# Kernel tuning notes

Hardware: AMD Instinct MI355X
Metric: run time of the kernel (lower is better)

## Reference

```python
import jax, jax.numpy as jnp
import numpy as np

NUM_PITCHES = 88
H_FEAT = 188
LSTM_UNITS = 48
N_STATES = 5
CTX_HID = 16
CTX_OUT = 4


def _glorot(key, shape):
    fan_in, fan_out = shape[1], shape[0]
    lim = (6.0 / (fan_in + fan_out)) ** 0.5
    return jax.random.uniform(key, shape, jnp.float32, -lim, lim)


def setup_inputs() -> dict:
    key = jax.random.key(0)
    ks = jax.random.split(key, 16)
    B, T = 16, 256
    pitch_features = jax.random.normal(ks[0], (B, NUM_PITCHES, H_FEAT, T), jnp.float32)
    prev_context = jax.random.uniform(ks[1], (B, NUM_PITCHES, 3), jnp.float32)
    # context net params
    fc1_w = _glorot(ks[2], (CTX_HID, 3)); fc1_b = jnp.zeros((CTX_HID,), jnp.float32)
    fc2_w = _glorot(ks[3], (CTX_HID, CTX_HID)); fc2_b = jnp.zeros((CTX_HID,), jnp.float32)
    fc3_w = _glorot(ks[4], (CTX_OUT, CTX_HID)); fc3_b = jnp.zeros((CTX_OUT,), jnp.float32)
    # lstm1: input H_FEAT+4 -> 48; gates order i,f,g,o (torch convention)
    in1 = H_FEAT + CTX_OUT
    lstm1_wih = _glorot(ks[5], (4 * LSTM_UNITS, in1))
    lstm1_whh = _glorot(ks[6], (4 * LSTM_UNITS, LSTM_UNITS))
    lstm1_bih = jnp.zeros((4 * LSTM_UNITS,), jnp.float32)
    lstm1_bhh = jnp.zeros((4 * LSTM_UNITS,), jnp.float32)
    lstm2_wih = _glorot(ks[7], (4 * LSTM_UNITS, LSTM_UNITS))
    lstm2_whh = _glorot(ks[8], (4 * LSTM_UNITS, LSTM_UNITS))
    lstm2_bih = jnp.zeros((4 * LSTM_UNITS,), jnp.float32)
    lstm2_bhh = jnp.zeros((4 * LSTM_UNITS,), jnp.float32)
    fc_states_w = _glorot(ks[9], (N_STATES, LSTM_UNITS))
    fc_states_b = jnp.zeros((N_STATES,), jnp.float32)
    return dict(pitch_features=pitch_features, prev_context=prev_context,
                fc1_w=fc1_w, fc1_b=fc1_b, fc2_w=fc2_w, fc2_b=fc2_b,
                fc3_w=fc3_w, fc3_b=fc3_b,
                lstm1_wih=lstm1_wih, lstm1_whh=lstm1_whh, lstm1_bih=lstm1_bih, lstm1_bhh=lstm1_bhh,
                lstm2_wih=lstm2_wih, lstm2_whh=lstm2_whh, lstm2_bih=lstm2_bih, lstm2_bhh=lstm2_bhh,
                fc_states_w=fc_states_w, fc_states_b=fc_states_b)


def _lstm_scan(x, wih, whh, bih, bhh):
    # x: (S, N, In); zero init state; returns (S, N, U)
    S, N, _ = x.shape
    U = whh.shape[1]
    xg = jnp.einsum('sni,gi->sng', x, wih) + bih + bhh  # precompute input gates

    def step(carry, xg_t):
        h, c = carry
        g = xg_t + h @ whh.T  # (N, 4U)
        i, f, gg, o = jnp.split(g, 4, axis=-1)
        c = jax.nn.sigmoid(f) * c + jax.nn.sigmoid(i) * jnp.tanh(gg)
        h = jax.nn.sigmoid(o) * jnp.tanh(c)
        return (h, c), h

    init = (jnp.zeros((N, U), x.dtype), jnp.zeros((N, U), x.dtype))
    _, hs = jax.lax.scan(step, init, xg)
    return hs


def reference(pitch_features, prev_context,
              fc1_w, fc1_b, fc2_w, fc2_b, fc3_w, fc3_b,
              lstm1_wih, lstm1_whh, lstm1_bih, lstm1_bhh,
              lstm2_wih, lstm2_whh, lstm2_bih, lstm2_bhh,
              fc_states_w, fc_states_b):
    B, P, H, T = pitch_features.shape
    # Context net (context never updates across t in the original loop)
    x = jax.nn.relu(prev_context @ fc1_w.T + fc1_b)
    x = jax.nn.relu(x @ fc2_w.T + fc2_b)
    ctx_emb = x @ fc3_w.T + fc3_b  # (B, P, 4)
    # Each timestep t is independent: LSTM runs over the pitch axis (len 88)
    # with zero initial state every step. Fold (B, T) into batch N.
    pf = jnp.transpose(pitch_features, (1, 0, 3, 2)).reshape(P, B * T, H)  # (P, BT, H)
    ce = jnp.broadcast_to(ctx_emb[:, None, :, :], (B, T, P, CTX_OUT))
    ce = jnp.transpose(ce, (2, 0, 1, 3)).reshape(P, B * T, CTX_OUT)
    seq = jnp.concatenate([pf, ce], axis=-1)  # (P, BT, H+4)
    h = _lstm_scan(seq, lstm1_wih, lstm1_whh, lstm1_bih, lstm1_bhh)
    h = _lstm_scan(h, lstm2_wih, lstm2_whh, lstm2_bih, lstm2_bhh)
    logits = h @ fc_states_w.T + fc_states_b  # (P, BT, 5)
    logits = logits.reshape(P, B, T, N_STATES)
    logits = jnp.transpose(logits, (1, 0, 3, 2))  # (B, P, 5, T)
    return jax.nn.softmax(logits, axis=2)
```

## Files before the change

kernel.cpp:

```cpp
#include <hip/hip_runtime.h>
#include <hip/hip_bf16.h>
#include <cstdint>

#define P_ 88
#define B_ 16
#define T_ 256
#define H_ 188
#define G_ 192
#define U_ 48
#define N_ 4096

typedef __attribute__((ext_vector_type(8))) short bf16x8;
typedef __attribute__((ext_vector_type(8))) _Float16 f16x8;
typedef __attribute__((ext_vector_type(4))) float f32x4;

__device__ __forceinline__ float sigf(float x) {
  return __builtin_amdgcn_rcpf(1.0f + __expf(-x));
}
__device__ __forceinline__ float tanh_f(float x) {
  return 1.0f - 2.0f * __builtin_amdgcn_rcpf(1.0f + __expf(2.0f * x));
}
__device__ __forceinline__ unsigned short f2bs(float v) {
  union { __hip_bfloat16 h; unsigned short s; } u;
  u.h = __float2bfloat16(v);
  return u.s;
}
__device__ __forceinline__ float bs2f(unsigned short s) {
  union { unsigned int u; float f; } x;
  x.u = ((unsigned int)s) << 16;
  return x.f;
}
__device__ __forceinline__ float hs2f(unsigned short s) {
  union { unsigned short u; _Float16 h; } x;
  x.u = s;
  return (float)x.h;
}
__device__ __forceinline__ unsigned short f2hs(float v) {
  union { _Float16 h; unsigned short s; } x;
  x.h = (_Float16)v;
  return x.s;
}

__device__ __forceinline__ void lds_barrier() {
  asm volatile("s_waitcnt lgkmcnt(0)\n\ts_barrier" ::: "memory");
}

__global__ void ctx_kernel(const float* __restrict__ pc,
                           const float* __restrict__ fc1w, const float* __restrict__ fc1b,
                           const float* __restrict__ fc2w, const float* __restrict__ fc2b,
                           const float* __restrict__ fc3w, const float* __restrict__ fc3b,
                           const float* __restrict__ wih1,
                           const float* __restrict__ bih1, const float* __restrict__ bhh1,
                           float* __restrict__ ctxg) {
  int bp = blockIdx.x * 64 + threadIdx.x;
  if (bp >= B_ * P_) return;
  float p0 = pc[bp * 3 + 0], p1 = pc[bp * 3 + 1], p2 = pc[bp * 3 + 2];
  float x1[16], x2[16];
#pragma unroll
  for (int jj = 0; jj < 16; ++jj)
    x1[jj] = fmaxf(0.f, fc1w[jj * 3 + 0] * p0 + fc1w[jj * 3 + 1] * p1 + fc1w[jj * 3 + 2] * p2 + fc1b[jj]);
#pragma unroll
  for (int jj = 0; jj < 16; ++jj) {
    float s = fc2b[jj];
#pragma unroll
    for (int i = 0; i < 16; ++i) s += fc2w[jj * 16 + i] * x1[i];
    x2[jj] = fmaxf(0.f, s);
  }
  float ce[4];
#pragma unroll
  for (int jj = 0; jj < 4; ++jj) {
    float s = fc3b[jj];
#pragma unroll
    for (int i = 0; i < 16; ++i) s += fc3w[jj * 16 + i] * x2[i];
    ce[jj] = s;
  }
  float* op = ctxg + (size_t)bp * G_;
  for (int g = 0; g < G_; ++g) {
    const float* wr = wih1 + (size_t)g * G_ + H_;
    op[g] = bih1[g] + bhh1[g] + ce[0] * wr[0] + ce[1] * wr[1] + ce[2] * wr[2] + ce[3] * wr[3];
  }
}

__global__ __launch_bounds__(256) void wfrag_kernel(const float* __restrict__ wih1,
                                                    f16x8* __restrict__ wfrag) {
  const int idx = blockIdx.x * 256 + threadIdx.x;
  if (idx >= 12 * 6 * 64) return;
  const int l = idx & 63;
  const int kc = (idx >> 6) % 6;
  const int j = idx / 384;
  const int g = j * 16 + (l & 15);
  const int k0 = kc * 32 + (l >> 4) * 8;
  f16x8 v;
#pragma unroll
  for (int e = 0; e < 8; ++e) {
    const int k = k0 + e;
    const float wv = (k < H_) ? wih1[(size_t)g * G_ + k] : 0.f;
    v[e] = (_Float16)wv;
  }
  wfrag[idx] = v;
}

__global__ __launch_bounds__(256, 3) void gemm_mfma(const float* __restrict__ pf,
                                                    const f16x8* __restrict__ wfrag,
                                                    const float* __restrict__ ctxg,
                                                    unsigned short* __restrict__ xg2) {
  const int bp = blockIdx.x >> 1, tb = blockIdx.x & 1;
  const int p = bp % P_, b = bp / P_;
  const int tid = threadIdx.x;
  const int w = tid >> 6, l = tid & 63;
  const int lj = l & 15, lq = l >> 4;

  __shared__ __align__(16) char ldsraw[49152];
  _Float16(*Ahi)[34] = (_Float16(*)[34])ldsraw;
  _Float16(*Alo)[34] = (_Float16(*)[34])(ldsraw + 8704);

  float cg[12];
#pragma unroll
  for (int jn = 0; jn < 12; ++jn)
    cg[jn] = ctxg[(size_t)bp * G_ + jn * 16 + lj];

  f32x4 acc[2][12];
#pragma unroll
  for (int mt = 0; mt < 2; ++mt)
#pragma unroll
    for (int jn = 0; jn < 12; ++jn)
#pragma unroll
      for (int r = 0; r < 4; ++r) acc[mt][jn][r] = 0.f;

  const float* Ab = pf + (size_t)bp * H_ * T_ + tb * 128;
  const int kl = tid >> 5;
  const int t4 = (tid & 31) * 4;

  for (int kc = 0; kc < 6; ++kc) {
    __syncthreads();
#pragma unroll
    for (int rr = 0; rr < 4; ++rr) {
      const int kk = rr * 8 + kl;
      const int kg = kc * 32 + kk;
      float a0 = 0.f, a1 = 0.f, a2 = 0.f, a3 = 0.f;
      if (kg < H_) {
        const float4 v = *(const float4*)(Ab + (size_t)kg * T_ + t4);
        a0 = v.x; a1 = v.y; a2 = v.z; a3 = v.w;
      }
      const _Float16 h0 = (_Float16)a0, h1 = (_Float16)a1;
      const _Float16 h2 = (_Float16)a2, h3 = (_Float16)a3;
      Ahi[t4 + 0][kk] = h0; Alo[t4 + 0][kk] = (_Float16)(a0 - (float)h0);
      Ahi[t4 + 1][kk] = h1; Alo[t4 + 1][kk] = (_Float16)(a1 - (float)h1);
      Ahi[t4 + 2][kk] = h2; Alo[t4 + 2][kk] = (_Float16)(a2 - (float)h2);
      Ahi[t4 + 3][kk] = h3; Alo[t4 + 3][kk] = (_Float16)(a3 - (float)h3);
    }
    __syncthreads();
    const int trow = w * 32;
    const f16x8 ahi0 = *(const f16x8*)&Ahi[trow + lj][lq * 8];
    const f16x8 ahi1 = *(const f16x8*)&Ahi[trow + 16 + lj][lq * 8];
    const f16x8 alo0 = *(const f16x8*)&Alo[trow + lj][lq * 8];
    const f16x8 alo1 = *(const f16x8*)&Alo[trow + 16 + lj][lq * 8];
#pragma unroll
    for (int jn = 0; jn < 12; ++jn) {
      const f16x8 wf = wfrag[(jn * 6 + kc) * 64 + l];
      acc[0][jn] = __builtin_amdgcn_mfma_f32_16x16x32_f16(ahi0, wf, acc[0][jn], 0, 0, 0);
      acc[1][jn] = __builtin_amdgcn_mfma_f32_16x16x32_f16(ahi1, wf, acc[1][jn], 0, 0, 0);
      acc[0][jn] = __builtin_amdgcn_mfma_f32_16x16x32_f16(alo0, wf, acc[0][jn], 0, 0, 0);
      acc[1][jn] = __builtin_amdgcn_mfma_f32_16x16x32_f16(alo1, wf, acc[1][jn], 0, 0, 0);
    }
  }
  __syncthreads();

  unsigned short* Cst = (unsigned short*)ldsraw + w * 6144;
#pragma unroll
  for (int mt = 0; mt < 2; ++mt)
#pragma unroll
    for (int jn = 0; jn < 12; ++jn)
#pragma unroll
      for (int r = 0; r < 4; ++r)
        Cst[mt * 3072 + jn * 256 + r * 64 + l] = f2hs(acc[mt][jn][r] + cg[jn]);
  const int nb0 = b * 16 + tb * 8 + w * 2;
  unsigned short* gb = xg2 + ((size_t)p * 256 + nb0) * 3072;
#pragma unroll
  for (int rr = 0; rr < 12; ++rr) {
    const uint4 v = *(const uint4*)(Cst + rr * 512 + l * 8);
    *(uint4*)(gb + rr * 512 + l * 8) = v;
  }
}

__global__ __launch_bounds__(256, 2) void scan_mfma(
    const unsigned short* __restrict__ xg2,
    const float* __restrict__ whh1, const float* __restrict__ wih2,
    const float* __restrict__ whh2, const float* __restrict__ bih2,
    const float* __restrict__ bhh2, const float* __restrict__ fcw,
    const float* __restrict__ fcb, float* __restrict__ out) {
  __shared__ __align__(16) short hh[16][104];
  __shared__ __align__(16) short hl[16][104];
  __shared__ __align__(16) float gs[8][196];
  __shared__ __align__(16) float h2f[8][52];
  __shared__ __align__(16) float fcws[5 * 48];
  __shared__ float logit_s[5][8];
  __shared__ float prob_s[5][8];

  const int tid = threadIdx.x;
  const int w = tid >> 6;
  const int l = tid & 63;
  const int lj = l & 15;
  const int lq = l >> 4;
  const int grp = blockIdx.x >> 1;
  const int half = blockIdx.x & 1;
  const int n0 = blockIdx.x * 8;
  const int b = n0 >> 8, t0 = n0 & 255;

  bf16x8 b1[3][2];
  bf16x8 b2f[3][3];
  float bias2r[3];
#pragma unroll
  for (int i = 0; i < 3; ++i) {
    const int j = w * 48 + i * 16 + lj;
    bias2r[i] = bih2[j] + bhh2[j];
#pragma unroll
    for (int kc = 0; kc < 2; ++kc)
#pragma unroll
      for (int e = 0; e < 8; ++e) {
        const int u = kc * 32 + lq * 8 + e;
        b1[i][kc][e] = (u < U_) ? (short)f2bs(whh1[j * U_ + u]) : (short)0;
      }
#pragma unroll
    for (int kc = 0; kc < 3; ++kc)
#pragma unroll
      for (int e = 0; e < 8; ++e) {
        const int u = kc * 32 + lq * 8 + e;
        b2f[i][kc][e] = (u < U_) ? (short)f2bs(wih2[j * U_ + u])
                                 : (short)f2bs(whh2[j * U_ + (u - U_)]);
      }
  }

  for (int e = tid; e < 16 * 104 / 2; e += 256) {
    ((unsigned int*)hh)[e] = 0u;
    ((unsigned int*)hl)[e] = 0u;
  }
  for (int e = tid; e < 5 * U_; e += 256) fcws[e] = fcw[e];

  const int tn0 = tid / U_, tu0 = tid % U_;
  const int tn1 = (256 + tid) / U_, tu1 = (256 + tid) % U_;
  float c1r[2] = {0.f, 0.f}, c2r[2] = {0.f, 0.f};
  const bool fcth = tid < 40;
  const int fk = tid >> 3, fn = tid & 7;
  const float fcbr = fcth ? fcb[fk] : 0.f;
  const int sk = (tid - 96) >> 3, sn = (tid - 96) & 7;

  unsigned short xp[12];
  {
    const size_t pb = (size_t)grp * 3072;
#pragma unroll
    for (int i = 0; i < 3; ++i)
#pragma unroll
      for (int r = 0; r < 4; ++r)
        xp[i * 4 + r] = (lq < 2)
            ? xg2[pb + (size_t)((w * 3 + i) * 256 + r * 64 + (half * 2 + lq) * 16 + lj)]
            : (unsigned short)0;
  }
  const short* hhrow = &hh[lj][0];
  const short* hlrow = &hl[lj][0];
  lds_barrier();

  for (int p = 0; p < P_; ++p) {
    f32x4 cH[3], cL[3];
#pragma unroll
    for (int i = 0; i < 3; ++i)
#pragma unroll
      for (int r = 0; r < 4; ++r) { cH[i][r] = hs2f(xp[i * 4 + r]); cL[i][r] = 0.f; }
    if (p < P_ - 1) {
      const size_t pb = (size_t)((p + 1) * 256 + grp) * 3072;
#pragma unroll
      for (int i = 0; i < 3; ++i)
#pragma unroll
        for (int r = 0; r < 4; ++r)
          xp[i * 4 + r] = (lq < 2)
              ? xg2[pb + (size_t)((w * 3 + i) * 256 + r * 64 + (half * 2 + lq) * 16 + lj)]
              : (unsigned short)0;
    }
    {
      bf16x8 ah0 = *(const bf16x8*)(hhrow + lq * 8);
      bf16x8 ah1 = *(const bf16x8*)(hhrow + 32 + lq * 8);
      bf16x8 al0 = *(const bf16x8*)(hlrow + lq * 8);
      bf16x8 al1 = *(const bf16x8*)(hlrow + 32 + lq * 8);
#pragma unroll
      for (int i = 0; i < 3; ++i)
        cH[i] = __builtin_amdgcn_mfma_f32_16x16x32_bf16(ah0, b1[i][0], cH[i], 0, 0, 0);
#pragma unroll
      for (int i = 0; i < 3; ++i)
        cL[i] = __builtin_amdgcn_mfma_f32_16x16x32_bf16(al0, b1[i][0], cL[i], 0, 0, 0);
#pragma unroll
      for (int i = 0; i < 3; ++i)
        cH[i] = __builtin_amdgcn_mfma_f32_16x16x32_bf16(ah1, b1[i][1], cH[i], 0, 0, 0);
#pragma unroll
      for (int i = 0; i < 3; ++i)
        cL[i] = __builtin_amdgcn_mfma_f32_16x16x32_bf16(al1, b1[i][1], cL[i], 0, 0, 0);
    }
    if (lq < 2) {
#pragma unroll
      for (int i = 0; i < 3; ++i)
#pragma unroll
        for (int r = 0; r < 4; ++r)
          gs[lq * 4 + r][w * 48 + i * 16 + lj] = cH[i][r] + cL[i][r];
    }
    if (p > 0 && fcth) {
      float a = fcbr;
#pragma unroll
      for (int uq = 0; uq < 12; ++uq) {
        f32x4 hv = *(const f32x4*)&h2f[fn][uq * 4];
        f32x4 wv = *(const f32x4*)&fcws[fk * 48 + uq * 4];
        a += hv[0] * wv[0] + hv[1] * wv[1] + hv[2] * wv[2] + hv[3] * wv[3];
      }
      logit_s[fk][fn] = a;
    }
    lds_barrier();
    {
      const int n = tn0, u = tu0;
      const float ig = gs[n][u], fg = gs[n][48 + u];
      const float gg = gs[n][96 + u], og = gs[n][144 + u];
      const float cc = sigf(fg) * c1r[0] + sigf(ig) * tanh_f(gg);
      c1r[0] = cc;
      const float h = sigf(og) * tanh_f(cc);
      const unsigned short hb = f2bs(h);
      hh[n][u] = (short)hb;
      hl[n][u] = (short)f2bs(h - bs2f(hb));
    }
    if (tid < 128) {
      const int n = tn1, u = tu1;
      const float ig = gs[n][u], fg = gs[n][48 + u];
      const float gg = gs[n][96 + u], og = gs[n][144 + u];
      const float cc = sigf(fg) * c1r[1] + sigf(ig) * tanh_f(gg);
      c1r[1] = cc;
      const float h = sigf(og) * tanh_f(cc);
      const unsigned short hb = f2bs(h);
      hh[n][u] = (short)hb;
      hl[n][u] = (short)f2bs(h - bs2f(hb));
    }
    if (p > 0 && tid >= 192 && tid < 200) {
      const int n = tid - 192;
      const float l0 = logit_s[0][n], l1 = logit_s[1][n], l2 = logit_s[2][n],
                  l3 = logit_s[3][n], l4 = logit_s[4][n];
      const float m = fmaxf(fmaxf(fmaxf(l0, l1), fmaxf(l2, l3)), l4);
      const float e0 = __expf(l0 - m), e1 = __expf(l1 - m), e2 = __expf(l2 - m),
                  e3 = __expf(l3 - m), e4 = __expf(l4 - m);
      const float rs = __builtin_amdgcn_rcpf(e0 + e1 + e2 + e3 + e4);
      prob_s[0][n] = e0 * rs; prob_s[1][n] = e1 * rs; prob_s[2][n] = e2 * rs;
      prob_s[3][n] = e3 * rs; prob_s[4][n] = e4 * rs;
    }
    lds_barrier();
    f32x4 c2H[3], c2L[3];
#pragma unroll
    for (int i = 0; i < 3; ++i) {
      c2H[i][0] = bias2r[i]; c2H[i][1] = bias2r[i];
      c2H[i][2] = bias2r[i]; c2H[i][3] = bias2r[i];
      c2L[i][0] = 0.f; c2L[i][1] = 0.f; c2L[i][2] = 0.f; c2L[i][3] = 0.f;
    }
    {
      bf16x8 a0 = *(const bf16x8*)(hhrow + lq * 8);
      bf16x8 a1 = *(const bf16x8*)(hhrow + 32 + lq * 8);
      bf16x8 a2 = *(const bf16x8*)(hhrow + 64 + lq * 8);
      bf16x8 q0 = *(const bf16x8*)(hlrow + lq * 8);
      bf16x8 q1 = *(const bf16x8*)(hlrow + 32 + lq * 8);
      bf16x8 q2 = *(const bf16x8*)(hlrow + 64 + lq * 8);
#pragma unroll
      for (int i = 0; i < 3; ++i)
        c2H[i] = __builtin_amdgcn_mfma_f32_16x16x32_bf16(a0, b2f[i][0], c2H[i], 0, 0, 0);
#pragma unroll
      for (int i = 0; i < 3; ++i)
        c2L[i] = __builtin_amdgcn_mfma_f32_16x16x32_bf16(q0, b2f[i][0], c2L[i], 0, 0, 0);
#pragma unroll
      for (int i = 0; i < 3; ++i)
        c2H[i] = __builtin_amdgcn_mfma_f32_16x16x32_bf16(a1, b2f[i][1], c2H[i], 0, 0, 0);
#pragma unroll
      for (int i = 0; i < 3; ++i)
        c2L[i] = __builtin_amdgcn_mfma_f32_16x16x32_bf16(q1, b2f[i][1], c2L[i], 0, 0, 0);
#pragma unroll
      for (int i = 0; i < 3; ++i)
        c2H[i] = __builtin_amdgcn_mfma_f32_16x16x32_bf16(a2, b2f[i][2], c2H[i], 0, 0, 0);
#pragma unroll
      for (int i = 0; i < 3; ++i)
        c2L[i] = __builtin_amdgcn_mfma_f32_16x16x32_bf16(q2, b2f[i][2], c2L[i], 0, 0, 0);
    }
    if (lq < 2) {
#pragma unroll
      for (int i = 0; i < 3; ++i)
#pragma unroll
        for (int r = 0; r < 4; ++r)
          gs[lq * 4 + r][w * 48 + i * 16 + lj] = c2H[i][r] + c2L[i][r];
    }
    if (p > 0 && tid >= 96 && tid < 136) {
      out[(((size_t)b * P_ + (p - 1)) * 5 + sk) * T_ + t0 + sn] = prob_s[sk][sn];
    }
    lds_barrier();
    {
      const int n = tn0, u = tu0;
      const float ig = gs[n][u], fg = gs[n][48 + u];
      const float gg = gs[n][96 + u], og = gs[n][144 + u];
      const float cc = sigf(fg) * c2r[0] + sigf(ig) * tanh_f(gg);
      c2r[0] = cc;
      const float h = sigf(og) * tanh_f(cc);
      const unsigned short hb = f2bs(h);
      hh[n][48 + u] = (short)hb;
      hl[n][48 + u] = (short)f2bs(h - bs2f(hb));
      h2f[n][u] = h;
    }
    if (tid < 128) {
      const int n = tn1, u = tu1;
      const float ig = gs[n][u], fg = gs[n][48 + u];
      const float gg = gs[n][96 + u], og = gs[n][144 + u];
      const float cc = sigf(fg) * c2r[1] + sigf(ig) * tanh_f(gg);
      c2r[1] = cc;
      const float h = sigf(og) * tanh_f(cc);
      const unsigned short hb = f2bs(h);
      hh[n][48 + u] = (short)hb;
      hl[n][48 + u] = (short)f2bs(h - bs2f(hb));
      h2f[n][u] = h;
    }
    lds_barrier();
  }
  if (fcth) {
    float a = fcbr;
#pragma unroll
    for (int uq = 0; uq < 12; ++uq) {
      f32x4 hv = *(const f32x4*)&h2f[fn][uq * 4];
      f32x4 wv = *(const f32x4*)&fcws[fk * 48 + uq * 4];
      a += hv[0] * wv[0] + hv[1] * wv[1] + hv[2] * wv[2] + hv[3] * wv[3];
    }
    logit_s[fk][fn] = a;
  }
  lds_barrier();
  if (tid >= 192 && tid < 200) {
    const int n = tid - 192;
    const float l0 = logit_s[0][n], l1 = logit_s[1][n], l2 = logit_s[2][n],
                l3 = logit_s[3][n], l4 = logit_s[4][n];
    const float m = fmaxf(fmaxf(fmaxf(l0, l1), fmaxf(l2, l3)), l4);
    const float e0 = __expf(l0 - m), e1 = __expf(l1 - m), e2 = __expf(l2 - m),
                e3 = __expf(l3 - m), e4 = __expf(l4 - m);
    const float rs = __builtin_amdgcn_rcpf(e0 + e1 + e2 + e3 + e4);
    prob_s[0][n] = e0 * rs; prob_s[1][n] = e1 * rs; prob_s[2][n] = e2 * rs;
    prob_s[3][n] = e3 * rs; prob_s[4][n] = e4 * rs;
  }
  lds_barrier();
  if (tid >= 96 && tid < 136) {
    out[(((size_t)b * P_ + (P_ - 1)) * 5 + sk) * T_ + t0 + sn] = prob_s[sk][sn];
  }
}

extern "C" void kernel_launch(void* const* d_in, const int* in_sizes, int n_in,
                              void* d_out, int out_size, void* d_ws, size_t ws_size,
                              hipStream_t stream) {
  const float* pf   = (const float*)d_in[0];
  const float* pc   = (const float*)d_in[1];
  const float* fc1w = (const float*)d_in[2];
  const float* fc1b = (const float*)d_in[3];
  const float* fc2w = (const float*)d_in[4];
  const float* fc2b = (const float*)d_in[5];
  const float* fc3w = (const float*)d_in[6];
  const float* fc3b = (const float*)d_in[7];
  const float* wih1 = (const float*)d_in[8];
  const float* whh1 = (const float*)d_in[9];
  const float* bih1 = (const float*)d_in[10];
  const float* bhh1 = (const float*)d_in[11];
  const float* wih2 = (const float*)d_in[12];
  const float* whh2 = (const float*)d_in[13];
  const float* bih2 = (const float*)d_in[14];
  const float* bhh2 = (const float*)d_in[15];
  const float* fcw  = (const float*)d_in[16];
  const float* fcb  = (const float*)d_in[17];
  float* out = (float*)d_out;

  char* wsp = (char*)d_ws;
  float* ctxg = (float*)wsp;
  const size_t CTXG_BYTES = (size_t)B_ * P_ * G_ * sizeof(float);
  f16x8* wfrag = (f16x8*)(wsp + CTXG_BYTES);
  const size_t WFRAG_BYTES = (size_t)12 * 6 * 64 * 16;
  unsigned short* xg2 = (unsigned short*)(wsp + CTXG_BYTES + WFRAG_BYTES);

  ctx_kernel<<<22, 64, 0, stream>>>(pc, fc1w, fc1b, fc2w, fc2b, fc3w, fc3b,
                                    wih1, bih1, bhh1, ctxg);
  wfrag_kernel<<<18, 256, 0, stream>>>(wih1, wfrag);
  gemm_mfma<<<B_ * P_ * 2, 256, 0, stream>>>(pf, wfrag, ctxg, xg2);
  scan_mfma<<<N_ / 8, 256, 0, stream>>>(xg2, whh1, wih2, whh2,
                                        bih2, bhh2, fcw, fcb, out);
}
```

Before: 413.2 us.

## Skew two LSTM layers into one wavefront loop and drop bf16 hi/lo split

```diff
diff --git a/kernel.cpp b/kernel.cpp
--- a/kernel.cpp
+++ b/kernel.cpp
@@ -19,16 +19,6 @@
 }
 __device__ __forceinline__ float tanh_f(float x) {
   return 1.0f - 2.0f * __builtin_amdgcn_rcpf(1.0f + __expf(2.0f * x));
-}
-__device__ __forceinline__ unsigned short f2bs(float v) {
-  union { __hip_bfloat16 h; unsigned short s; } u;
-  u.h = __float2bfloat16(v);
-  return u.s;
-}
-__device__ __forceinline__ float bs2f(unsigned short s) {
-  union { unsigned int u; float f; } x;
-  x.u = ((unsigned int)s) << 16;
-  return x.f;
 }
 __device__ __forceinline__ float hs2f(unsigned short s) {
   union { unsigned short u; _Float16 h; } x;
@@ -189,9 +179,9 @@
     const float* __restrict__ whh2, const float* __restrict__ bih2,
     const float* __restrict__ bhh2, const float* __restrict__ fcw,
     const float* __restrict__ fcb, float* __restrict__ out) {
-  __shared__ __align__(16) short hh[16][104];
-  __shared__ __align__(16) short hl[16][104];
-  __shared__ __align__(16) float gs[8][196];
+  __shared__ __align__(16) _Float16 h12[16][104];
+  __shared__ __align__(16) float gs1[8][196];
+  __shared__ __align__(16) float gs2[8][196];
   __shared__ __align__(16) float h2f[8][52];
   __shared__ __align__(16) float fcws[5 * 48];
   __shared__ float logit_s[5][8];
@@ -207,8 +197,8 @@
   const int n0 = blockIdx.x * 8;
   const int b = n0 >> 8, t0 = n0 & 255;
 
-  bf16x8 b1[3][2];
-  bf16x8 b2f[3][3];
+  f16x8 b1[3][2];
+  f16x8 b2f[3][3];
   float bias2r[3];
 #pragma unroll
   for (int i = 0; i < 3; ++i) {
@@ -219,31 +209,33 @@
 #pragma unroll
       for (int e = 0; e < 8; ++e) {
         const int u = kc * 32 + lq * 8 + e;
-        b1[i][kc][e] = (u < U_) ? (short)f2bs(whh1[j * U_ + u]) : (short)0;
+        b1[i][kc][e] = (u < U_) ? (_Float16)whh1[j * U_ + u] : (_Float16)0.f;
       }
 #pragma unroll
     for (int kc = 0; kc < 3; ++kc)
 #pragma unroll
       for (int e = 0; e < 8; ++e) {
-        const int u = kc * 32 + lq * 8 + e;
-        b2f[i][kc][e] = (u < U_) ? (short)f2bs(wih2[j * U_ + u])
-                                 : (short)f2bs(whh2[j * U_ + (u - U_)]);
-      }
-  }
-
-  for (int e = tid; e < 16 * 104 / 2; e += 256) {
-    ((unsigned int*)hh)[e] = 0u;
-    ((unsigned int*)hl)[e] = 0u;
-  }
+        const int k = kc * 32 + lq * 8 + e;
+        b2f[i][kc][e] = (k < U_) ? (_Float16)wih2[j * U_ + k]
+                                 : (_Float16)whh2[j * U_ + (k - U_)];
+      }
+  }
+
+  for (int e = tid; e < 16 * 104 / 2; e += 256) ((unsigned int*)h12)[e] = 0u;
   for (int e = tid; e < 5 * U_; e += 256) fcws[e] = fcw[e];
 
   const int tn0 = tid / U_, tu0 = tid % U_;
   const int tn1 = (256 + tid) / U_, tu1 = (256 + tid) % U_;
-  float c1r[2] = {0.f, 0.f}, c2r[2] = {0.f, 0.f};
+  const bool has2 = (tid < 128);
+  float c1s[2] = {0.f, 0.f}, c2s[2] = {0.f, 0.f};
+
   const bool fcth = tid < 40;
   const int fk = tid >> 3, fn = tid & 7;
   const float fcbr = fcth ? fcb[fk] : 0.f;
+  const bool stth = tid >= 96 && tid < 136;
   const int sk = (tid - 96) >> 3, sn = (tid - 96) & 7;
+  const bool smth = tid >= 192 && tid < 200;
+  const int smn = tid - 192;
 
   unsigned short xp[12];
   {
@@ -256,52 +248,38 @@
             ? xg2[pb + (size_t)((w * 3 + i) * 256 + r * 64 + (half * 2 + lq) * 16 + lj)]
             : (unsigned short)0;
   }
-  const short* hhrow = &hh[lj][0];
-  const short* hlrow = &hl[lj][0];
   lds_barrier();
 
-  for (int p = 0; p < P_; ++p) {
-    f32x4 cH[3], cL[3];
-#pragma unroll
-    for (int i = 0; i < 3; ++i)
-#pragma unroll
-      for (int r = 0; r < 4; ++r) { cH[i][r] = hs2f(xp[i * 4 + r]); cL[i][r] = 0.f; }
-    if (p < P_ - 1) {
-      const size_t pb = (size_t)((p + 1) * 256 + grp) * 3072;
-#pragma unroll
-      for (int i = 0; i < 3; ++i)
-#pragma unroll
-        for (int r = 0; r < 4; ++r)
-          xp[i * 4 + r] = (lq < 2)
-              ? xg2[pb + (size_t)((w * 3 + i) * 256 + r * 64 + (half * 2 + lq) * 16 + lj)]
-              : (unsigned short)0;
-    }
-    {
-      bf16x8 ah0 = *(const bf16x8*)(hhrow + lq * 8);
-      bf16x8 ah1 = *(const bf16x8*)(hhrow + 32 + lq * 8);
-      bf16x8 al0 = *(const bf16x8*)(hlrow + lq * 8);
-      bf16x8 al1 = *(const bf16x8*)(hlrow + 32 + lq * 8);
-#pragma unroll
-      for (int i = 0; i < 3; ++i)
-        cH[i] = __builtin_amdgcn_mfma_f32_16x16x32_bf16(ah0, b1[i][0], cH[i], 0, 0, 0);
-#pragma unroll
-      for (int i = 0; i < 3; ++i)
-        cL[i] = __builtin_amdgcn_mfma_f32_16x16x32_bf16(al0, b1[i][0], cL[i], 0, 0, 0);
-#pragma unroll
-      for (int i = 0; i < 3; ++i)
-        cH[i] = __builtin_amdgcn_mfma_f32_16x16x32_bf16(ah1, b1[i][1], cH[i], 0, 0, 0);
-#pragma unroll
-      for (int i = 0; i < 3; ++i)
-        cL[i] = __builtin_amdgcn_mfma_f32_16x16x32_bf16(al1, b1[i][1], cL[i], 0, 0, 0);
-    }
-    if (lq < 2) {
-#pragma unroll
-      for (int i = 0; i < 3; ++i)
-#pragma unroll
-        for (int r = 0; r < 4; ++r)
-          gs[lq * 4 + r][w * 48 + i * 16 + lj] = cH[i][r] + cL[i][r];
-    }
-    if (p > 0 && fcth) {
+  for (int p = -1; p < P_; ++p) {
+    const _Float16* hr = &h12[lj][0];
+    const f16x8 f0 = *(const f16x8*)(hr + lq * 8);
+    const f16x8 f1 = *(const f16x8*)(hr + 32 + lq * 8);
+    const f16x8 f2 = *(const f16x8*)(hr + 64 + lq * 8);
+    if (p >= 0) {
+      f32x4 dH[3];
+#pragma unroll
+      for (int i = 0; i < 3; ++i) {
+        dH[i][0] = bias2r[i]; dH[i][1] = bias2r[i];
+        dH[i][2] = bias2r[i]; dH[i][3] = bias2r[i];
+      }
+#pragma unroll
+      for (int i = 0; i < 3; ++i)
+        dH[i] = __builtin_amdgcn_mfma_f32_16x16x32_f16(f0, b2f[i][0], dH[i], 0, 0, 0);
+#pragma unroll
+      for (int i = 0; i < 3; ++i)
+        dH[i] = __builtin_amdgcn_mfma_f32_16x16x32_f16(f1, b2f[i][1], dH[i], 0, 0, 0);
+#pragma unroll
+      for (int i = 0; i < 3; ++i)
+        dH[i] = __builtin_amdgcn_mfma_f32_16x16x32_f16(f2, b2f[i][2], dH[i], 0, 0, 0);
+      if (lq < 2) {
+#pragma unroll
+        for (int i = 0; i < 3; ++i)
+#pragma unroll
+          for (int r = 0; r < 4; ++r)
+            gs2[lq * 4 + r][w * 48 + i * 16 + lj] = dH[i][r];
+      }
+    }
+    if (p >= 1 && fcth) {
       float a = fcbr;
 #pragma unroll
       for (int uq = 0; uq < 12; ++uq) {
@@ -311,31 +289,83 @@
       }
       logit_s[fk][fn] = a;
     }
+    if (p >= 2 && stth) {
+      out[(((size_t)b * P_ + (p - 2)) * 5 + sk) * T_ + t0 + sn] = prob_s[sk][sn];
+    }
+    __builtin_amdgcn_sched_barrier(0);
+    if (p < P_ - 1) {
+      f32x4 cH[3];
+#pragma unroll
+      for (int i = 0; i < 3; ++i)
+#pragma unroll
+        for (int r = 0; r < 4; ++r) cH[i][r] = hs2f(xp[i * 4 + r]);
+      if (p < P_ - 2) {
+        const size_t pb = (size_t)((p + 2) * 256 + grp) * 3072;
+#pragma unroll
+        for (int i = 0; i < 3; ++i)
+#pragma unroll
+          for (int r = 0; r < 4; ++r)
+            xp[i * 4 + r] = (lq < 2)
+                ? xg2[pb + (size_t)((w * 3 + i) * 256 + r * 64 + (half * 2 + lq) * 16 + lj)]
+                : (unsigned short)0;
+      }
+#pragma unroll
+      for (int i = 0; i < 3; ++i)
+        cH[i] = __builtin_amdgcn_mfma_f32_16x16x32_f16(f0, b1[i][0], cH[i], 0, 0, 0);
+#pragma unroll
+      for (int i = 0; i < 3; ++i)
+        cH[i] = __builtin_amdgcn_mfma_f32_16x16x32_f16(f1, b1[i][1], cH[i], 0, 0, 0);
+      if (lq < 2) {
+#pragma unroll
+        for (int i = 0; i < 3; ++i)
+#pragma unroll
+          for (int r = 0; r < 4; ++r)
+            gs1[lq * 4 + r][w * 48 + i * 16 + lj] = cH[i][r];
+      }
+    }
     lds_barrier();
-    {
-      const int n = tn0, u = tu0;
-      const float ig = gs[n][u], fg = gs[n][48 + u];
-      const float gg = gs[n][96 + u], og = gs[n][144 + u];
-      const float cc = sigf(fg) * c1r[0] + sigf(ig) * tanh_f(gg);
-      c1r[0] = cc;
-      const float h = sigf(og) * tanh_f(cc);
-      const unsigned short hb = f2bs(h);
-      hh[n][u] = (short)hb;
-      hl[n][u] = (short)f2bs(h - bs2f(hb));
-    }
-    if (tid < 128) {
-      const int n = tn1, u = tu1;
-      const float ig = gs[n][u], fg = gs[n][48 + u];
-      const float gg = gs[n][96 + u], og = gs[n][144 + u];
-      const float cc = sigf(fg) * c1r[1] + sigf(ig) * tanh_f(gg);
-      c1r[1] = cc;
-      const float h = sigf(og) * tanh_f(cc);
-      const unsigned short hb = f2bs(h);
-      hh[n][u] = (short)hb;
-      hl[n][u] = (short)f2bs(h - bs2f(hb));
-    }
-    if (p > 0 && tid >= 192 && tid < 200) {
-      const int n = tid - 192;
+    if (p >= 0) {
+      {
+        const int n = tn0, u = tu0;
+        const float ig = gs2[n][u], fg = gs2[n][48 + u];
+        const float gg = gs2[n][96 + u], og = gs2[n][144 + u];
+        const float cc = sigf(fg) * c2s[0] + sigf(ig) * tanh_f(gg);
+        c2s[0] = cc;
+        const float h = sigf(og) * tanh_f(cc);
+        h12[n][48 + u] = (_Float16)h;
+        h2f[n][u] = h;
+      }
+      if (has2) {
+        const int n = tn1, u = tu1;
+        const float ig = gs2[n][u], fg = gs2[n][48 + u];
+        const float gg = gs2[n][96 + u], og = gs2[n][144 + u];
+        const float cc = sigf(fg) * c2s[1] + sigf(ig) * tanh_f(gg);
+        c2s[1] = cc;
+        const float h = sigf(og) * tanh_f(cc);
+        h12[n][48 + u] = (_Float16)h;
+        h2f[n][u] = h;
+      }
+    }
+    if (p < P_ - 1) {
+      {
+        const int n = tn0, u = tu0;
+        const float ig = gs1[n][u], fg = gs1[n][48 + u];
+        const float gg = gs1[n][96 + u], og = gs1[n][144 + u];
+        const float cc = sigf(fg) * c1s[0] + sigf(ig) * tanh_f(gg);
+        c1s[0] = cc;
+        h12[n][u] = (_Float16)(sigf(og) * tanh_f(cc));
+      }
+      if (has2) {
+        const int n = tn1, u = tu1;
+        const float ig = gs1[n][u], fg = gs1[n][48 + u];
+        const float gg = gs1[n][96 + u], og = gs1[n][144 + u];
+        const float cc = sigf(fg) * c1s[1] + sigf(ig) * tanh_f(gg);
+        c1s[1] = cc;
+        h12[n][u] = (_Float16)(sigf(og) * tanh_f(cc));
+      }
+    }
+    if (p >= 1 && smth) {
+      const int n = smn;
       const float l0 = logit_s[0][n], l1 = logit_s[1][n], l2 = logit_s[2][n],
                   l3 = logit_s[3][n], l4 = logit_s[4][n];
       const float m = fmaxf(fmaxf(fmaxf(l0, l1), fmaxf(l2, l3)), l4);
@@ -346,75 +376,6 @@
       prob_s[3][n] = e3 * rs; prob_s[4][n] = e4 * rs;
     }
     lds_barrier();
-    f32x4 c2H[3], c2L[3];
-#pragma unroll
-    for (int i = 0; i < 3; ++i) {
-      c2H[i][0] = bias2r[i]; c2H[i][1] = bias2r[i];
-      c2H[i][2] = bias2r[i]; c2H[i][3] = bias2r[i];
-      c2L[i][0] = 0.f; c2L[i][1] = 0.f; c2L[i][2] = 0.f; c2L[i][3] = 0.f;
-    }
-    {
-      bf16x8 a0 = *(const bf16x8*)(hhrow + lq * 8);
-      bf16x8 a1 = *(const bf16x8*)(hhrow + 32 + lq * 8);
-      bf16x8 a2 = *(const bf16x8*)(hhrow + 64 + lq * 8);
-      bf16x8 q0 = *(const bf16x8*)(hlrow + lq * 8);
-      bf16x8 q1 = *(const bf16x8*)(hlrow + 32 + lq * 8);
-      bf16x8 q2 = *(const bf16x8*)(hlrow + 64 + lq * 8);
-#pragma unroll
-      for (int i = 0; i < 3; ++i)
-        c2H[i] = __builtin_amdgcn_mfma_f32_16x16x32_bf16(a0, b2f[i][0], c2H[i], 0, 0, 0);
-#pragma unroll
-      for (int i = 0; i < 3; ++i)
-        c2L[i] = __builtin_amdgcn_mfma_f32_16x16x32_bf16(q0, b2f[i][0], c2L[i], 0, 0, 0);
-#pragma unroll
-      for (int i = 0; i < 3; ++i)
-        c2H[i] = __builtin_amdgcn_mfma_f32_16x16x32_bf16(a1, b2f[i][1], c2H[i], 0, 0, 0);
-#pragma unroll
-      for (int i = 0; i < 3; ++i)
-        c2L[i] = __builtin_amdgcn_mfma_f32_16x16x32_bf16(q1, b2f[i][1], c2L[i], 0, 0, 0);
-#pragma unroll
-      for (int i = 0; i < 3; ++i)
-        c2H[i] = __builtin_amdgcn_mfma_f32_16x16x32_bf16(a2, b2f[i][2], c2H[i], 0, 0, 0);
-#pragma unroll
-      for (int i = 0; i < 3; ++i)
-        c2L[i] = __builtin_amdgcn_mfma_f32_16x16x32_bf16(q2, b2f[i][2], c2L[i], 0, 0, 0);
-    }
-    if (lq < 2) {
-#pragma unroll
-      for (int i = 0; i < 3; ++i)
-#pragma unroll
-        for (int r = 0; r < 4; ++r)
-          gs[lq * 4 + r][w * 48 + i * 16 + lj] = c2H[i][r] + c2L[i][r];
-    }
-    if (p > 0 && tid >= 96 && tid < 136) {
-      out[(((size_t)b * P_ + (p - 1)) * 5 + sk) * T_ + t0 + sn] = prob_s[sk][sn];
-    }
-    lds_barrier();
-    {
-      const int n = tn0, u = tu0;
-      const float ig = gs[n][u], fg = gs[n][48 + u];
-      const float gg = gs[n][96 + u], og = gs[n][144 + u];
-      const float cc = sigf(fg) * c2r[0] + sigf(ig) * tanh_f(gg);
-      c2r[0] = cc;
-      const float h = sigf(og) * tanh_f(cc);
-      const unsigned short hb = f2bs(h);
-      hh[n][48 + u] = (short)hb;
-      hl[n][48 + u] = (short)f2bs(h - bs2f(hb));
-      h2f[n][u] = h;
-    }
-    if (tid < 128) {
-      const int n = tn1, u = tu1;
-      const float ig = gs[n][u], fg = gs[n][48 + u];
-      const float gg = gs[n][96 + u], og = gs[n][144 + u];
-      const float cc = sigf(fg) * c2r[1] + sigf(ig) * tanh_f(gg);
-      c2r[1] = cc;
-      const float h = sigf(og) * tanh_f(cc);
-      const unsigned short hb = f2bs(h);
-      hh[n][48 + u] = (short)hb;
-      hl[n][48 + u] = (short)f2bs(h - bs2f(hb));
-      h2f[n][u] = h;
-    }
-    lds_barrier();
   }
   if (fcth) {
     float a = fcbr;
@@ -426,9 +387,12 @@
     }
     logit_s[fk][fn] = a;
   }
+  if (stth) {
+    out[(((size_t)b * P_ + (P_ - 2)) * 5 + sk) * T_ + t0 + sn] = prob_s[sk][sn];
+  }
   lds_barrier();
-  if (tid >= 192 && tid < 200) {
-    const int n = tid - 192;
+  if (smth) {
+    const int n = smn;
     const float l0 = logit_s[0][n], l1 = logit_s[1][n], l2 = logit_s[2][n],
                 l3 = logit_s[3][n], l4 = logit_s[4][n];
     const float m = fmaxf(fmaxf(fmaxf(l0, l1), fmaxf(l2, l3)), l4);
@@ -439,7 +403,7 @@
     prob_s[3][n] = e3 * rs; prob_s[4][n] = e4 * rs;
   }
   lds_barrier();
-  if (tid >= 96 && tid < 136) {
+  if (stth) {
     out[(((size_t)b * P_ + (P_ - 1)) * 5 + sk) * T_ + t0 + sn] = prob_s[sk][sn];
   }
 }
```

Result: faster. 397.2 us (-3.9%).
